# Kernel tuning notes

Measured on AMD Instinct MI355X. Metric: run time of the kernel, lower is better.

Reference implementation:

```python
import jax, jax.numpy as jnp
import numpy as np

D_MODEL = 256
N_HEAD = 8
D_FF = 2048
B, N = 8, 1024
NEG = -9e15
EPS = 1e-5


def _layernorm(x, g, b):
    mu = jnp.mean(x, axis=-1, keepdims=True)
    var = jnp.mean(jnp.square(x - mu), axis=-1, keepdims=True)
    return (x - mu) * jax.lax.rsqrt(var + EPS) * g + b


def setup_inputs() -> dict:
    key = jax.random.key(0)
    ks = jax.random.split(key, 12)
    d, dff = D_MODEL, D_FF
    s = 1.0 / np.sqrt(d)
    inp = {
        "src": jax.random.normal(ks[0], (B, N, d), dtype=jnp.float32),
        "adj": jax.random.randint(ks[1], (B, N, N), 0, 2, dtype=jnp.int32),
        "W_gat": jax.random.normal(ks[2], (d, d), dtype=jnp.float32) * s,
        "a_gat": jax.random.normal(ks[3], (2 * d, 1), dtype=jnp.float32) * s,
        "in_proj_w": jax.random.normal(ks[4], (3 * d, d), dtype=jnp.float32) * s,
        "in_proj_b": jnp.zeros((3 * d,), dtype=jnp.float32),
        "out_proj_w": jax.random.normal(ks[5], (d, d), dtype=jnp.float32) * s,
        "out_proj_b": jnp.zeros((d,), dtype=jnp.float32),
        "lin1_w": jax.random.normal(ks[6], (dff, d), dtype=jnp.float32) * s,
        "lin1_b": jnp.zeros((dff,), dtype=jnp.float32),
        "lin2_w": jax.random.normal(ks[7], (d, dff), dtype=jnp.float32) * (1.0 / np.sqrt(dff)),
        "lin2_b": jnp.zeros((d,), dtype=jnp.float32),
        "ln1_g": jnp.ones((d,), dtype=jnp.float32),
        "ln1_b": jnp.zeros((d,), dtype=jnp.float32),
        "ln2_g": jnp.ones((d,), dtype=jnp.float32),
        "ln2_b": jnp.zeros((d,), dtype=jnp.float32),
        "ln3_g": jnp.ones((d,), dtype=jnp.float32),
        "ln3_b": jnp.zeros((d,), dtype=jnp.float32),
    }
    return inp


def reference(src, adj, W_gat, a_gat, in_proj_w, in_proj_b, out_proj_w, out_proj_b,
              lin1_w, lin1_b, lin2_w, lin2_b, ln1_g, ln1_b, ln2_g, ln2_b, ln3_g, ln3_b):
    d = D_MODEL
    # --- Graph attention (dropout inactive in eval) ---
    Wh = jnp.matmul(src, W_gat)                      # [B,N,d]
    a1 = a_gat[:d, 0]
    a2 = a_gat[d:, 0]
    # e[b,i,j] = Wh_i . a1 + Wh_j . a2  (equivalent to concat+matmul in source)
    f1 = Wh @ a1                                     # [B,N]
    f2 = Wh @ a2                                     # [B,N]
    e = f1[:, :, None] + f2[:, None, :]              # [B,N,N]
    e = jnp.where(adj > 0, e, NEG)
    attn = jax.nn.softmax(e, axis=-1)
    h_prime = jnp.matmul(attn, Wh)                   # [B,N,d]
    graph_out = jax.nn.elu(h_prime)
    x = _layernorm(src + graph_out, ln1_g, ln1_b)

    # --- Multi-head self-attention ---
    qkv = x @ in_proj_w.T + in_proj_b                # [B,N,3d]
    q, k, v = jnp.split(qkv, 3, axis=-1)
    hd = d // N_HEAD
    def heads(t):
        return t.reshape(B, N, N_HEAD, hd).transpose(0, 2, 1, 3)  # [B,H,N,hd]
    q, k, v = heads(q), heads(k), heads(v)
    scores = jnp.einsum("bhid,bhjd->bhij", q, k) / np.sqrt(hd)
    probs = jax.nn.softmax(scores, axis=-1)
    ctx = jnp.einsum("bhij,bhjd->bhid", probs, v)
    ctx = ctx.transpose(0, 2, 1, 3).reshape(B, N, d)
    attn_out = ctx @ out_proj_w.T + out_proj_b
    y = _layernorm(x + attn_out, ln2_g, ln2_b)

    # --- FFN ---
    ff = jax.nn.relu(y @ lin1_w.T + lin1_b) @ lin2_w.T + lin2_b
    return _layernorm(y + ff, ln3_g, ln3_b)
```

## Files before the change

kernel.cpp:

```cpp
#include <hip/hip_runtime.h>
#include <math.h>

constexpr int BATCH = 8;
constexpr int SEQ   = 1024;
constexpr int DM    = 256;
constexpr int DF    = 2048;
constexpr int NH    = 8;
constexpr int HDIM  = 32;
constexpr int ROWS  = BATCH * SEQ;
constexpr float NEGV = -9e15f;
constexpr float EPSV = 1e-5f;
constexpr float QSCALE = 0.2550351822f;
constexpr float LOG2E  = 1.44269504f;

typedef __attribute__((ext_vector_type(8))) short short8;
typedef __attribute__((ext_vector_type(4))) float f32x4;

static __device__ __forceinline__ ushort f2bf(float f) {
    unsigned x = __float_as_uint(f);
    unsigned r = (x + 0x7fffu + ((x >> 16) & 1u)) >> 16;
    return (ushort)r;
}
static __device__ __forceinline__ unsigned cvt_pk_bf16(float lo, float hi) {
    unsigned r;
    asm volatile("v_cvt_pk_bf16_f32 %0, %1, %2" : "=v"(r) : "v"(lo), "v"(hi));
    return r;
}
static __device__ __forceinline__ void gl16(const ushort* g, ushort* l) {
    __builtin_amdgcn_global_load_lds(
        (const __attribute__((address_space(1))) void*)g,
        (__attribute__((address_space(3))) void*)l, 16, 0, 0);
}

struct CastArgs {
    const float* in[5];
    ushort* out[5];
    int n4[5];
};
__global__ __launch_bounds__(256) void castall_k(CastArgs a)
{
    int idx = blockIdx.x * 256 + threadIdx.x;
    #pragma unroll
    for (int r = 0; r < 5; r++) {
        if (idx < a.n4[r]) {
            float4 v = *(const float4*)&a.in[r][(size_t)idx * 4];
            ushort4 o; o.x = f2bf(v.x); o.y = f2bf(v.y); o.z = f2bf(v.z); o.w = f2bf(v.w);
            *(ushort4*)&a.out[r][(size_t)idx * 4] = o;
            return;
        }
        idx -= a.n4[r];
    }
}

__global__ __launch_bounds__(256) void tcast_k(const float* __restrict__ In,
                                               ushort* __restrict__ Out,
                                               int R, int C)
{
    __shared__ float Ts[32][33];
    const int r0 = blockIdx.y * 32, c0 = blockIdx.x * 32;
    const int t = threadIdx.x;
    const int lr = t >> 3, lc4 = (t & 7) * 4;
    float4 v = *(const float4*)&In[(size_t)(r0 + lr) * C + c0 + lc4];
    Ts[lr][lc4] = v.x; Ts[lr][lc4 + 1] = v.y; Ts[lr][lc4 + 2] = v.z; Ts[lr][lc4 + 3] = v.w;
    __syncthreads();
    const int oc = t >> 3, or4 = (t & 7) * 4;
    ushort4 o;
    o.x = f2bf(Ts[or4 + 0][oc]); o.y = f2bf(Ts[or4 + 1][oc]);
    o.z = f2bf(Ts[or4 + 2][oc]); o.w = f2bf(Ts[or4 + 3][oc]);
    *(ushort4*)&Out[(size_t)(c0 + oc) * R + r0 + or4] = o;
}

__global__ __launch_bounds__(256) void w12_k(const float* __restrict__ W_gat,
                                             const float* __restrict__ a_gat,
                                             float* __restrict__ w1,
                                             float* __restrict__ w2)
{
    const int t = threadIdx.x;
    const int k = blockIdx.x * 4 + (t >> 6);
    const int l = t & 63;
    float4 wv = *(const float4*)&W_gat[(size_t)k * DM + 4 * l];
    float4 a1 = *(const float4*)&a_gat[4 * l];
    float4 a2 = *(const float4*)&a_gat[DM + 4 * l];
    float s1 = wv.x*a1.x + wv.y*a1.y + wv.z*a1.z + wv.w*a1.w;
    float s2 = wv.x*a2.x + wv.y*a2.y + wv.z*a2.z + wv.w*a2.w;
    #pragma unroll
    for (int off = 32; off; off >>= 1) {
        s1 += __shfl_xor(s1, off, 64);
        s2 += __shfl_xor(s2, off, 64);
    }
    if (l == 0) { w1[k] = s1; w2[k] = s2; }
}

__global__ __launch_bounds__(256) void f12_k(const float* __restrict__ src,
                                             const float* __restrict__ w1,
                                             const float* __restrict__ w2,
                                             float* __restrict__ f1,
                                             float* __restrict__ f2)
{
    const int t = threadIdx.x;
    const size_t row = (size_t)blockIdx.x * 4 + (t >> 6);
    const int l = t & 63;
    float s1 = 0.f, s2 = 0.f;
    #pragma unroll
    for (int i = 0; i < 4; i++) {
        float v = src[row * DM + l + 64*i];
        s1 = fmaf(v, w1[l + 64*i], s1);
        s2 = fmaf(v, w2[l + 64*i], s2);
    }
    #pragma unroll
    for (int off = 32; off; off >>= 1) {
        s1 += __shfl_xor(s1, off, 64);
        s2 += __shfl_xor(s2, off, 64);
    }
    if (l == 0) { f1[row] = s1 * LOG2E; f2[row] = s2 * LOG2E; }
}

template<int EP, int BM, int BN>
__global__ __launch_bounds__(256) void gemm_bf(const ushort* __restrict__ A,
                                               const ushort* __restrict__ B,
                                               const float* __restrict__ bias,
                                               float* __restrict__ Cf,
                                               ushort* __restrict__ Cb,
                                               int M, int N, int K, int ldB,
                                               long long sA, long long sB, long long sC)
{
    __shared__ ushort As[2][BM][32];
    __shared__ ushort Bs[2][BN][32];
    A += (size_t)blockIdx.z * sA;
    B += (size_t)blockIdx.z * sB;

    const int t  = threadIdx.x;
    const int m0 = blockIdx.y * BM, n0 = blockIdx.x * BN;
    const int lane = t & 63, lo = lane & 15, hi = lane >> 4;
    const int w = t >> 6;
    constexpr int NI = BM / 32, NJ = BN / 32;
    const int wr = (w >> 1) * (BM / 2);
    const int wc = (w & 1) * (BN / 2);

    const int lr16 = lane >> 2;
    const int lc8  = (lane & 3) * 8;

    f32x4 acc[NI][NJ];
    const f32x4 zero = {0.f, 0.f, 0.f, 0.f};
    #pragma unroll
    for (int i = 0; i < NI; i++)
        #pragma unroll
        for (int j = 0; j < NJ; j++) acc[i][j] = zero;

    auto stage = [&](int buf, int k0) {
        if constexpr (BM == 128) {
            gl16(A + (size_t)(m0 + 32*w      + lr16) * K + k0 + lc8, &As[buf][32*w][0]);
            gl16(A + (size_t)(m0 + 32*w + 16 + lr16) * K + k0 + lc8, &As[buf][32*w + 16][0]);
        } else {
            gl16(A + (size_t)(m0 + 16*w + lr16) * K + k0 + lc8, &As[buf][16*w][0]);
        }
        if constexpr (BN == 128) {
            gl16(B + (size_t)(n0 + 32*w      + lr16) * ldB + k0 + lc8, &Bs[buf][32*w][0]);
            gl16(B + (size_t)(n0 + 32*w + 16 + lr16) * ldB + k0 + lc8, &Bs[buf][32*w + 16][0]);
        } else {
            gl16(B + (size_t)(n0 + 16*w + lr16) * ldB + k0 + lc8, &Bs[buf][16*w][0]);
        }
    };

    stage(0, 0);
    const int NT = K >> 5;
    for (int it = 0; it < NT; it++) {
        const int cur = it & 1;
        __syncthreads();
        if (it + 1 < NT) stage(cur ^ 1, (it + 1) << 5);

        short8 afr[NI], bfr[NJ];
        #pragma unroll
        for (int i = 0; i < NI; i++) afr[i] = *(const short8*)&As[cur][wr + i*16 + lo][hi * 8];
        #pragma unroll
        for (int j = 0; j < NJ; j++) bfr[j] = *(const short8*)&Bs[cur][wc + j*16 + lo][hi * 8];
        #pragma unroll
        for (int i = 0; i < NI; i++)
            #pragma unroll
            for (int j = 0; j < NJ; j++)
                acc[i][j] = __builtin_amdgcn_mfma_f32_16x16x32_bf16(afr[i], bfr[j], acc[i][j], 0, 0, 0);
    }

    if (EP == 2 || EP == 5 || EP == 6) Cb += (size_t)blockIdx.z * sC;
    else                               Cf += (size_t)blockIdx.z * sC;
    #pragma unroll
    for (int j = 0; j < NJ; j++) {
        const int col = n0 + wc + j * 16 + lo;
        float bj = (EP == 1 || EP == 2 || EP == 6) ? bias[col] : 0.f;
        #pragma unroll
        for (int i = 0; i < NI; i++) {
            const int rbase = m0 + wr + i * 16 + hi * 4;
            #pragma unroll
            for (int r = 0; r < 4; r++) {
                float v = acc[i][j][r] + bj;
                if (EP == 3) v = v > 0.f ? v : expm1f(v);
                if (EP == 2) v = fmaxf(v, 0.f);
                if (EP == 6 && col < DM) v *= QSCALE;
                if (EP == 2 || EP == 5 || EP == 6) Cb[(size_t)(rbase + r) * N + col] = f2bf(v);
                else                               Cf[(size_t)(rbase + r) * N + col] = v;
            }
        }
    }
}

template<bool WB>
__global__ __launch_bounds__(256) void ln_k(const float* __restrict__ a,
                                            const float* __restrict__ r,
                                            const float* __restrict__ g,
                                            const float* __restrict__ be,
                                            float* __restrict__ o,
                                            ushort* __restrict__ ob)
{
    const size_t row = (size_t)blockIdx.x * 4 + (threadIdx.x >> 6);
    const int l = threadIdx.x & 63;
    const float* pa = a + row * DM;
    const float* pr = r + row * DM;
    float v[4]; float s = 0.f;
    #pragma unroll
    for (int i = 0; i < 4; i++) { v[i] = pa[l + 64*i] + pr[l + 64*i]; s += v[i]; }
    #pragma unroll
    for (int off = 32; off; off >>= 1) s += __shfl_xor(s, off, 64);
    float mu = s * (1.0f / DM);
    float q = 0.f;
    #pragma unroll
    for (int i = 0; i < 4; i++) { float d = v[i] - mu; q += d * d; }
    #pragma unroll
    for (int off = 32; off; off >>= 1) q += __shfl_xor(q, off, 64);
    float rs = rsqrtf(q * (1.0f / DM) + EPSV);
    #pragma unroll
    for (int i = 0; i < 4; i++) {
        int c = l + 64*i;
        float out = (v[i] - mu) * rs * g[c] + be[c];
        o[row * DM + c] = out;
        if (WB) ob[row * DM + c] = f2bf(out);
    }
}

__global__ __launch_bounds__(256) void gat_sm_k(const int* __restrict__ adj,
                                                const float* __restrict__ f1,
                                                const float* __restrict__ f2,
                                                ushort* __restrict__ P)
{
    __shared__ float red[8];
    const int i = blockIdx.x, b = i >> 10;
    const int t = threadIdx.x;
    const int4 a4 = *(const int4*)&adj[(size_t)i * SEQ + 4 * t];
    const float4 f4 = *(const float4*)&f2[(size_t)(b << 10) + 4 * t];
    const float f1i = f1[i];
    float e[4];
    e[0] = a4.x > 0 ? f1i + f4.x : NEGV;
    e[1] = a4.y > 0 ? f1i + f4.y : NEGV;
    e[2] = a4.z > 0 ? f1i + f4.z : NEGV;
    e[3] = a4.w > 0 ? f1i + f4.w : NEGV;
    float mx = fmaxf(fmaxf(e[0], e[1]), fmaxf(e[2], e[3]));
    #pragma unroll
    for (int off = 32; off; off >>= 1) mx = fmaxf(mx, __shfl_xor(mx, off, 64));
    if ((t & 63) == 0) red[t >> 6] = mx;
    __syncthreads();
    mx = fmaxf(fmaxf(red[0], red[1]), fmaxf(red[2], red[3]));
    float s = 0.f;
    #pragma unroll
    for (int u = 0; u < 4; u++) { e[u] = exp2f(e[u] - mx); s += e[u]; }
    #pragma unroll
    for (int off = 32; off; off >>= 1) s += __shfl_xor(s, off, 64);
    if ((t & 63) == 0) red[4 + (t >> 6)] = s;
    __syncthreads();
    float inv = 1.0f / (red[4] + red[5] + red[6] + red[7]);
    ushort4 o;
    o.x = f2bf(e[0] * inv); o.y = f2bf(e[1] * inv);
    o.z = f2bf(e[2] * inv); o.w = f2bf(e[3] * inv);
    *(ushort4*)&P[(size_t)i * SEQ + 4 * t] = o;
}

__device__ __forceinline__ int vt_idx(int d, int kv) { return d * 72 + ((d >> 3) & 3) * 16 + kv; }
constexpr int VTSZ = 32 * 72 + 3 * 16 + 8;

__global__ __launch_bounds__(256) void mha_k(const ushort* __restrict__ qkv,
                                             ushort* __restrict__ ctxb)
{
    __shared__ ushort Ks[2][64][40];
    __shared__ ushort Vt[2][VTSZ];
    __shared__ ushort Ps[64][72];

    const int blk = blockIdx.x;
    const int qt = blk & 15, h = (blk >> 4) & 7, b = blk >> 7;
    const int i0 = qt << 6;
    const int t = threadIdx.x;
    const int w = t >> 6, lane = t & 63, lo = lane & 15, hi = lane >> 4;
    const int gsh = lane & 48;
    const size_t base = (size_t)b * SEQ * 768;

    const short8 aQ = *(const short8*)(qkv + base + (size_t)(i0 + 16*w + lo) * 768 + h * HDIM + hi * 8);
    short8 ones;
    #pragma unroll
    for (int e = 0; e < 8; e++) ones[e] = (short)0x3F80;

    const int srow = t >> 2, scb = (t & 3) << 3;
    const int vcol = (srow & 32) | ((srow & 15) << 1) | ((srow >> 4) & 1);
    {
        const ushort* p0 = qkv + base + (size_t)srow * 768 + h * HDIM;
        short8 k0 = *(const short8*)(p0 + 256 + scb);
        short8 v0 = *(const short8*)(p0 + 512 + scb);
        *(short8*)&Ks[0][srow][scb] = k0;
        #pragma unroll
        for (int e = 0; e < 8; e++) Vt[0][vt_idx(scb + e, vcol)] = (ushort)v0[e];
    }

    float m_run[4], l_run[4];
    f32x4 O0 = {0.f, 0.f, 0.f, 0.f}, O1 = {0.f, 0.f, 0.f, 0.f};
    #pragma unroll
    for (int r = 0; r < 4; r++) { m_run[r] = -3.0e38f; l_run[r] = 0.f; }
    const f32x4 zero = {0.f, 0.f, 0.f, 0.f};

    short8 kreg, vreg;
    for (int it = 0; it < 16; it++) {
        const int cur = it & 1;
        if (it < 15) {
            const ushort* nb = qkv + base + (size_t)((it + 1) * 64 + srow) * 768 + h * HDIM;
            kreg = *(const short8*)(nb + 256 + scb);
            vreg = *(const short8*)(nb + 512 + scb);
        }
        __syncthreads();

        f32x4 S[4];
        #pragma unroll
        for (int jt = 0; jt < 4; jt++) {
            short8 bK = *(const short8*)&Ks[cur][16 * jt + lo][hi * 8];
            S[jt] = __builtin_amdgcn_mfma_f32_16x16x32_bf16(aQ, bK, zero, 0, 0, 0);
        }

        float mxl[4];
        bool any = false;
        #pragma unroll
        for (int r = 0; r < 4; r++) {
            mxl[r] = fmaxf(fmaxf(S[0][r], S[1][r]), fmaxf(S[2][r], S[3][r]));
            any = any || (mxl[r] > m_run[r] + 8.f);
        }
        unsigned long long bal = __ballot(any);
        if ((bal >> gsh) & 0xffffULL) {
            #pragma unroll
            for (int r = 0; r < 4; r++) {
                float mx = mxl[r];
                #pragma unroll
                for (int off = 8; off; off >>= 1) mx = fmaxf(mx, __shfl_xor(mx, off, 16));
                float mnew = fmaxf(m_run[r], mx);
                float sc = exp2f(m_run[r] - mnew);
                m_run[r] = mnew;
                l_run[r] *= sc; O0[r] *= sc; O1[r] *= sc;
            }
        }
        #pragma unroll
        for (int r = 0; r < 4; r++) {
            const int row = 16 * w + 4 * hi + r;
            unsigned u01 = cvt_pk_bf16(exp2f(S[0][r] - m_run[r]), exp2f(S[1][r] - m_run[r]));
            unsigned u23 = cvt_pk_bf16(exp2f(S[2][r] - m_run[r]), exp2f(S[3][r] - m_run[r]));
            *(unsigned*)&Ps[row][2 * lo]      = u01;
            *(unsigned*)&Ps[row][32 + 2 * lo] = u23;
        }

        f32x4 O2 = zero;
        #pragma unroll
        for (int kt = 0; kt < 2; kt++) {
            short8 aP  = *(const short8*)&Ps[16 * w + lo][32 * kt + hi * 8];
            short8 bV0 = *(const short8*)&Vt[cur][vt_idx(lo,      32 * kt + hi * 8)];
            short8 bV1 = *(const short8*)&Vt[cur][vt_idx(16 + lo, 32 * kt + hi * 8)];
            O0 = __builtin_amdgcn_mfma_f32_16x16x32_bf16(aP, bV0, O0, 0, 0, 0);
            O1 = __builtin_amdgcn_mfma_f32_16x16x32_bf16(aP, bV1, O1, 0, 0, 0);
            O2 = __builtin_amdgcn_mfma_f32_16x16x32_bf16(aP, ones, O2, 0, 0, 0);
        }
        #pragma unroll
        for (int r = 0; r < 4; r++) l_run[r] += O2[r];

        if (it < 15) {
            *(short8*)&Ks[cur ^ 1][srow][scb] = kreg;
            #pragma unroll
            for (int e = 0; e < 8; e++) Vt[cur ^ 1][vt_idx(scb + e, vcol)] = (ushort)vreg[e];
        }
    }

    #pragma unroll
    for (int r = 0; r < 4; r++) {
        float inv = 1.0f / l_run[r];
        size_t row = (size_t)b * SEQ + i0 + 16 * w + 4 * hi + r;
        ctxb[row * DM + h * HDIM + lo]      = f2bf(O0[r] * inv);
        ctxb[row * DM + h * HDIM + 16 + lo] = f2bf(O1[r] * inv);
    }
}

extern "C" void kernel_launch(void* const* d_in, const int* in_sizes, int n_in,
                              void* d_out, int out_size, void* d_ws, size_t ws_size,
                              hipStream_t stream)
{
    const float* src        = (const float*)d_in[0];
    const int*   adj        = (const int*)  d_in[1];
    const float* W_gat      = (const float*)d_in[2];
    const float* a_gat      = (const float*)d_in[3];
    const float* in_proj_w  = (const float*)d_in[4];
    const float* in_proj_b  = (const float*)d_in[5];
    const float* out_proj_w = (const float*)d_in[6];
    const float* out_proj_b = (const float*)d_in[7];
    const float* lin1_w     = (const float*)d_in[8];
    const float* lin1_b     = (const float*)d_in[9];
    const float* lin2_w     = (const float*)d_in[10];
    const float* lin2_b     = (const float*)d_in[11];
    const float* ln1_g      = (const float*)d_in[12];
    const float* ln1_b_     = (const float*)d_in[13];
    const float* ln2_g      = (const float*)d_in[14];
    const float* ln2_b_     = (const float*)d_in[15];
    const float* ln3_g      = (const float*)d_in[16];
    const float* ln3_b_     = (const float*)d_in[17];

    char* base = (char*)d_ws;
    const size_t MB = 1024 * 1024;
    float*  tmp   = (float*) (base + 0 * MB);
    float*  x     = (float*) (base + 8 * MB);
    float*  y     = (float*) (base + 16 * MB);
    ushort* P_bf  = (ushort*)(base + 24 * MB);
    ushort* qkvb  = (ushort*)(base + 24 * MB);
    ushort* ff1b  = (ushort*)(base + 24 * MB);
    ushort* srcb  = (ushort*)(base + 56 * MB);
    ushort* WhTb  = (ushort*)(base + 60 * MB);
    ushort* xb    = (ushort*)(base + 64 * MB);
    ushort* yb    = (ushort*)(base + 68 * MB);
    ushort* ctxb  = (ushort*)(base + 72 * MB);
    float*  f1    = (float*) (base + 76 * MB);
    float*  f2    = f1 + ROWS;
    float*  w1    = f2 + ROWS;
    float*  w2    = w1 + DM;
    ushort* wgTb  = (ushort*)(base + 77 * MB);
    ushort* ipwb  = wgTb + 65536;
    ushort* opwb  = ipwb + 196608;
    ushort* l1wb  = opwb + 65536;
    ushort* l2wb  = l1wb + 524288;

    dim3 b256(256);

    CastArgs ca;
    ca.in[0] = src;       ca.out[0] = srcb; ca.n4[0] = 2097152 / 4;
    ca.in[1] = in_proj_w; ca.out[1] = ipwb; ca.n4[1] = 196608 / 4;
    ca.in[2] = out_proj_w;ca.out[2] = opwb; ca.n4[2] = 65536 / 4;
    ca.in[3] = lin1_w;    ca.out[3] = l1wb; ca.n4[3] = 524288 / 4;
    ca.in[4] = lin2_w;    ca.out[4] = l2wb; ca.n4[4] = 524288 / 4;
    castall_k<<<(2097152 + 196608 + 65536 + 524288 + 524288) / 4 / 256, b256, 0, stream>>>(ca);
    tcast_k<<<dim3(8, 8), b256, 0, stream>>>(W_gat, wgTb, 256, 256);

    w12_k<<<64, b256, 0, stream>>>(W_gat, a_gat, w1, w2);
    f12_k<<<ROWS / 4, b256, 0, stream>>>(src, w1, w2, f1, f2);
    gemm_bf<5, 64, 64><<<dim3(ROWS/64, DM/64, 1), b256, 0, stream>>>(wgTb, srcb, nullptr, nullptr, WhTb,
                                                                     DM, ROWS, DM, DM, 0, 0, 0);
    gat_sm_k<<<ROWS, b256, 0, stream>>>(adj, f1, f2, P_bf);
    gemm_bf<3, 64, 64><<<dim3(DM/64, SEQ/64, 8), b256, 0, stream>>>(P_bf, WhTb, nullptr, tmp, nullptr,
                                                                    SEQ, DM, SEQ, ROWS,
                                                                    (long long)SEQ * SEQ, (long long)SEQ, (long long)SEQ * DM);
    ln_k<true><<<ROWS / 4, b256, 0, stream>>>(src, tmp, ln1_g, ln1_b_, x, xb);

    gemm_bf<6, 128, 64><<<dim3(768/64, ROWS/128, 1), b256, 0, stream>>>(xb, ipwb, in_proj_b, nullptr, qkvb,
                                                                        ROWS, 768, DM, DM, 0, 0, 0);
    mha_k<<<BATCH * NH * (SEQ / 64), b256, 0, stream>>>(qkvb, ctxb);
    gemm_bf<1, 64, 64><<<dim3(DM/64, ROWS/64, 1), b256, 0, stream>>>(ctxb, opwb, out_proj_b, tmp, nullptr,
                                                                     ROWS, DM, DM, DM, 0, 0, 0);
    ln_k<true><<<ROWS / 4, b256, 0, stream>>>(x, tmp, ln2_g, ln2_b_, y, yb);

    gemm_bf<2, 128, 128><<<dim3(DF/128, ROWS/128, 1), b256, 0, stream>>>(yb, l1wb, lin1_b, nullptr, ff1b,
                                                                         ROWS, DF, DM, DM, 0, 0, 0);
    gemm_bf<1, 64, 64><<<dim3(DM/64, ROWS/64, 1), b256, 0, stream>>>(ff1b, l2wb, lin2_b, tmp, nullptr,
                                                                     ROWS, DM, DF, DF, 0, 0, 0);
    ln_k<false><<<ROWS / 4, b256, 0, stream>>>(y, tmp, ln3_g, ln3_b_, (float*)d_out, nullptr);
}
```

Measured before the change: 169.4 us.

## Fuse residual-add LayerNorm into epilogues of N=256 GEMMs

Adds a gemm_ln_k kernel in which each block computes a full 32x256 output row-tile, stages it through shared memory, then applies the bias/ELU, residual add and LayerNorm in place. It replaces the three GEMM + separate ln_k pairs: GAT aggregation, out-projection and FFN down-projection. This removes the fp32 tmp round-trip and three launches. The trade-off is far fewer blocks (256 per launch) and a larger shared-memory footprint, so the K=2048 FFN down-projection in particular may lose parallelism.

```diff
diff --git a/kernel.cpp b/kernel.cpp
--- a/kernel.cpp
+++ b/kernel.cpp
@@ -119,15 +119,11 @@
 __global__ __launch_bounds__(256) void gemm_bf(const ushort* __restrict__ A,
                                                const ushort* __restrict__ B,
                                                const float* __restrict__ bias,
-                                               float* __restrict__ Cf,
                                                ushort* __restrict__ Cb,
-                                               int M, int N, int K, int ldB,
-                                               long long sA, long long sB, long long sC)
+                                               int N, int K, int ldB)
 {
     __shared__ ushort As[2][BM][32];
     __shared__ ushort Bs[2][BN][32];
-    A += (size_t)blockIdx.z * sA;
-    B += (size_t)blockIdx.z * sB;
 
     const int t  = threadIdx.x;
     const int m0 = blockIdx.y * BM, n0 = blockIdx.x * BN;
@@ -181,58 +177,147 @@
                 acc[i][j] = __builtin_amdgcn_mfma_f32_16x16x32_bf16(afr[i], bfr[j], acc[i][j], 0, 0, 0);
     }
 
-    if (EP == 2 || EP == 5 || EP == 6) Cb += (size_t)blockIdx.z * sC;
-    else                               Cf += (size_t)blockIdx.z * sC;
     #pragma unroll
     for (int j = 0; j < NJ; j++) {
         const int col = n0 + wc + j * 16 + lo;
-        float bj = (EP == 1 || EP == 2 || EP == 6) ? bias[col] : 0.f;
+        float bj = (EP == 2 || EP == 6) ? bias[col] : 0.f;
         #pragma unroll
         for (int i = 0; i < NI; i++) {
             const int rbase = m0 + wr + i * 16 + hi * 4;
             #pragma unroll
             for (int r = 0; r < 4; r++) {
                 float v = acc[i][j][r] + bj;
-                if (EP == 3) v = v > 0.f ? v : expm1f(v);
                 if (EP == 2) v = fmaxf(v, 0.f);
                 if (EP == 6 && col < DM) v *= QSCALE;
-                if (EP == 2 || EP == 5 || EP == 6) Cb[(size_t)(rbase + r) * N + col] = f2bf(v);
-                else                               Cf[(size_t)(rbase + r) * N + col] = v;
+                Cb[(size_t)(rbase + r) * N + col] = f2bf(v);
             }
         }
     }
 }
 
-template<bool WB>
-__global__ __launch_bounds__(256) void ln_k(const float* __restrict__ a,
-                                            const float* __restrict__ r,
-                                            const float* __restrict__ g,
-                                            const float* __restrict__ be,
-                                            float* __restrict__ o,
-                                            ushort* __restrict__ ob)
-{
-    const size_t row = (size_t)blockIdx.x * 4 + (threadIdx.x >> 6);
-    const int l = threadIdx.x & 63;
-    const float* pa = a + row * DM;
-    const float* pr = r + row * DM;
-    float v[4]; float s = 0.f;
-    #pragma unroll
-    for (int i = 0; i < 4; i++) { v[i] = pa[l + 64*i] + pr[l + 64*i]; s += v[i]; }
-    #pragma unroll
-    for (int off = 32; off; off >>= 1) s += __shfl_xor(s, off, 64);
-    float mu = s * (1.0f / DM);
-    float q = 0.f;
-    #pragma unroll
-    for (int i = 0; i < 4; i++) { float d = v[i] - mu; q += d * d; }
-    #pragma unroll
-    for (int off = 32; off; off >>= 1) q += __shfl_xor(q, off, 64);
-    float rs = rsqrtf(q * (1.0f / DM) + EPSV);
-    #pragma unroll
-    for (int i = 0; i < 4; i++) {
-        int c = l + 64*i;
-        float out = (v[i] - mu) * rs * g[c] + be[c];
-        o[row * DM + c] = out;
-        if (WB) ob[row * DM + c] = f2bf(out);
+template<int ACT, bool WB>
+__global__ __launch_bounds__(256) void gemm_ln_k(const ushort* __restrict__ A,
+                                                 const ushort* __restrict__ B,
+                                                 const float* __restrict__ bias,
+                                                 const float* __restrict__ resid,
+                                                 const float* __restrict__ g,
+                                                 const float* __restrict__ be,
+                                                 float* __restrict__ outF,
+                                                 ushort* __restrict__ outB,
+                                                 int K, int ldB,
+                                                 long long sA, long long sB, long long sR)
+{
+    union U {
+        struct { ushort As[2][32][32]; ushort Bs[2][256][32]; } s;
+        float vals[32][264];
+    };
+    __shared__ U u;
+
+    A     += (size_t)blockIdx.z * sA;
+    B     += (size_t)blockIdx.z * sB;
+    resid += (size_t)blockIdx.z * sR;
+    outF  += (size_t)blockIdx.z * sR;
+    if (WB) outB += (size_t)blockIdx.z * sR;
+
+    const int t = threadIdx.x;
+    const int m0 = blockIdx.y * 32;
+    const int lane = t & 63, lo = lane & 15, hi = lane >> 4;
+    const int w = t >> 6;
+    const int lr16 = lane >> 2, lc8 = (lane & 3) * 8;
+
+    f32x4 acc[2][4];
+    const f32x4 zero = {0.f, 0.f, 0.f, 0.f};
+    #pragma unroll
+    for (int i = 0; i < 2; i++)
+        #pragma unroll
+        for (int j = 0; j < 4; j++) acc[i][j] = zero;
+
+    auto stage = [&](int buf, int k0) {
+        if (w < 2)
+            gl16(A + (size_t)(m0 + 16*w + lr16) * K + k0 + lc8, &u.s.As[buf][16*w][0]);
+        #pragma unroll
+        for (int j = 0; j < 4; j++)
+            gl16(B + (size_t)(j*64 + 16*w + lr16) * ldB + k0 + lc8, &u.s.Bs[buf][j*64 + 16*w][0]);
+    };
+
+    stage(0, 0);
+    const int NT = K >> 5;
+    for (int it = 0; it < NT; it++) {
+        const int cur = it & 1;
+        __syncthreads();
+        if (it + 1 < NT) stage(cur ^ 1, (it + 1) << 5);
+
+        short8 afr[2], bfr[4];
+        #pragma unroll
+        for (int i = 0; i < 2; i++) afr[i] = *(const short8*)&u.s.As[cur][i*16 + lo][hi * 8];
+        #pragma unroll
+        for (int j = 0; j < 4; j++) bfr[j] = *(const short8*)&u.s.Bs[cur][64*w + j*16 + lo][hi * 8];
+        #pragma unroll
+        for (int i = 0; i < 2; i++)
+            #pragma unroll
+            for (int j = 0; j < 4; j++)
+                acc[i][j] = __builtin_amdgcn_mfma_f32_16x16x32_bf16(afr[i], bfr[j], acc[i][j], 0, 0, 0);
+    }
+
+    __syncthreads();
+
+    #pragma unroll
+    for (int j = 0; j < 4; j++) {
+        const int col = 64*w + j*16 + lo;
+        float bj = (ACT == 1) ? bias[col] : 0.f;
+        #pragma unroll
+        for (int i = 0; i < 2; i++) {
+            const int rbase = i*16 + hi*4;
+            #pragma unroll
+            for (int r = 0; r < 4; r++) {
+                float v = acc[i][j][r] + bj;
+                if (ACT == 0) v = v > 0.f ? v : expm1f(v);
+                u.vals[rbase + r][col] = v;
+            }
+        }
+    }
+    __syncthreads();
+
+    const int row = t >> 3, s = t & 7;
+    const float* rrow = resid + (size_t)(m0 + row) * DM + s * 32;
+    float vv[32];
+    float sum = 0.f;
+    #pragma unroll
+    for (int q = 0; q < 8; q++) {
+        float4 rv = *(const float4*)(rrow + 4*q);
+        vv[4*q+0] = u.vals[row][s*32 + 4*q + 0] + rv.x;
+        vv[4*q+1] = u.vals[row][s*32 + 4*q + 1] + rv.y;
+        vv[4*q+2] = u.vals[row][s*32 + 4*q + 2] + rv.z;
+        vv[4*q+3] = u.vals[row][s*32 + 4*q + 3] + rv.w;
+        sum += (vv[4*q] + vv[4*q+1]) + (vv[4*q+2] + vv[4*q+3]);
+    }
+    #pragma unroll
+    for (int off = 1; off < 8; off <<= 1) sum += __shfl_xor(sum, off, 8);
+    const float mu = sum * (1.0f / DM);
+    float qs = 0.f;
+    #pragma unroll
+    for (int k = 0; k < 32; k++) { float d = vv[k] - mu; qs += d * d; }
+    #pragma unroll
+    for (int off = 1; off < 8; off <<= 1) qs += __shfl_xor(qs, off, 8);
+    const float rs = rsqrtf(qs * (1.0f / DM) + EPSV);
+
+    float* orow = outF + (size_t)(m0 + row) * DM + s * 32;
+    #pragma unroll
+    for (int q = 0; q < 8; q++) {
+        const int c = s*32 + 4*q;
+        float4 gv = *(const float4*)&g[c];
+        float4 bv = *(const float4*)&be[c];
+        float4 o;
+        o.x = (vv[4*q+0] - mu) * rs * gv.x + bv.x;
+        o.y = (vv[4*q+1] - mu) * rs * gv.y + bv.y;
+        o.z = (vv[4*q+2] - mu) * rs * gv.z + bv.z;
+        o.w = (vv[4*q+3] - mu) * rs * gv.w + bv.w;
+        *(float4*)(orow + 4*q) = o;
+        if (WB) {
+            ushort4 ob;
+            ob.x = f2bf(o.x); ob.y = f2bf(o.y); ob.z = f2bf(o.z); ob.w = f2bf(o.w);
+            *(ushort4*)&outB[(size_t)(m0 + row) * DM + c] = ob;
+        }
     }
 }
 
@@ -412,22 +497,21 @@
 
     char* base = (char*)d_ws;
     const size_t MB = 1024 * 1024;
-    float*  tmp   = (float*) (base + 0 * MB);
-    float*  x     = (float*) (base + 8 * MB);
-    float*  y     = (float*) (base + 16 * MB);
-    ushort* P_bf  = (ushort*)(base + 24 * MB);
-    ushort* qkvb  = (ushort*)(base + 24 * MB);
-    ushort* ff1b  = (ushort*)(base + 24 * MB);
-    ushort* srcb  = (ushort*)(base + 56 * MB);
-    ushort* WhTb  = (ushort*)(base + 60 * MB);
-    ushort* xb    = (ushort*)(base + 64 * MB);
-    ushort* yb    = (ushort*)(base + 68 * MB);
-    ushort* ctxb  = (ushort*)(base + 72 * MB);
-    float*  f1    = (float*) (base + 76 * MB);
+    float*  x     = (float*) (base + 0 * MB);
+    float*  y     = (float*) (base + 8 * MB);
+    ushort* P_bf  = (ushort*)(base + 16 * MB);
+    ushort* qkvb  = (ushort*)(base + 16 * MB);
+    ushort* ff1b  = (ushort*)(base + 16 * MB);
+    ushort* srcb  = (ushort*)(base + 48 * MB);
+    ushort* WhTb  = (ushort*)(base + 52 * MB);
+    ushort* xb    = (ushort*)(base + 56 * MB);
+    ushort* yb    = (ushort*)(base + 60 * MB);
+    ushort* ctxb  = (ushort*)(base + 64 * MB);
+    float*  f1    = (float*) (base + 68 * MB);
     float*  f2    = f1 + ROWS;
     float*  w1    = f2 + ROWS;
     float*  w2    = w1 + DM;
-    ushort* wgTb  = (ushort*)(base + 77 * MB);
+    ushort* wgTb  = (ushort*)(base + 69 * MB);
     ushort* ipwb  = wgTb + 65536;
     ushort* opwb  = ipwb + 196608;
     ushort* l1wb  = opwb + 65536;
@@ -446,24 +530,24 @@
 
     w12_k<<<64, b256, 0, stream>>>(W_gat, a_gat, w1, w2);
     f12_k<<<ROWS / 4, b256, 0, stream>>>(src, w1, w2, f1, f2);
-    gemm_bf<5, 64, 64><<<dim3(ROWS/64, DM/64, 1), b256, 0, stream>>>(wgTb, srcb, nullptr, nullptr, WhTb,
-                                                                     DM, ROWS, DM, DM, 0, 0, 0);
+    gemm_bf<5, 64, 64><<<dim3(ROWS/64, DM/64, 1), b256, 0, stream>>>(wgTb, srcb, nullptr, WhTb,
+                                                                     ROWS, DM, DM);
     gat_sm_k<<<ROWS, b256, 0, stream>>>(adj, f1, f2, P_bf);
-    gemm_bf<3, 64, 64><<<dim3(DM/64, SEQ/64, 8), b256, 0, stream>>>(P_bf, WhTb, nullptr, tmp, nullptr,
-                                                                    SEQ, DM, SEQ, ROWS,
-                                                                    (long long)SEQ * SEQ, (long long)SEQ, (long long)SEQ * DM);
-    ln_k<true><<<ROWS / 4, b256, 0, stream>>>(src, tmp, ln1_g, ln1_b_, x, xb);
-
-    gemm_bf<6, 128, 64><<<dim3(768/64, ROWS/128, 1), b256, 0, stream>>>(xb, ipwb, in_proj_b, nullptr, qkvb,
-                                                                        ROWS, 768, DM, DM, 0, 0, 0);
+    gemm_ln_k<0, true><<<dim3(1, SEQ/32, 8), b256, 0, stream>>>(P_bf, WhTb, nullptr,
+                                                                src, ln1_g, ln1_b_, x, xb,
+                                                                SEQ, ROWS,
+                                                                (long long)SEQ * SEQ, (long long)SEQ, (long long)SEQ * DM);
+
+    gemm_bf<6, 128, 64><<<dim3(768/64, ROWS/128, 1), b256, 0, stream>>>(xb, ipwb, in_proj_b, qkvb,
+                                                                        768, DM, DM);
     mha_k<<<BATCH * NH * (SEQ / 64), b256, 0, stream>>>(qkvb, ctxb);
-    gemm_bf<1, 64, 64><<<dim3(DM/64, ROWS/64, 1), b256, 0, stream>>>(ctxb, opwb, out_proj_b, tmp, nullptr,
-                                                                     ROWS, DM, DM, DM, 0, 0, 0);
-    ln_k<true><<<ROWS / 4, b256, 0, stream>>>(x, tmp, ln2_g, ln2_b_, y, yb);
-
-    gemm_bf<2, 128, 128><<<dim3(DF/128, ROWS/128, 1), b256, 0, stream>>>(yb, l1wb, lin1_b, nullptr, ff1b,
-                                                                         ROWS, DF, DM, DM, 0, 0, 0);
-    gemm_bf<1, 64, 64><<<dim3(DM/64, ROWS/64, 1), b256, 0, stream>>>(ff1b, l2wb, lin2_b, tmp, nullptr,
-                                                                     ROWS, DM, DF, DF, 0, 0, 0);
-    ln_k<false><<<ROWS / 4, b256, 0, stream>>>(y, tmp, ln3_g, ln3_b_, (float*)d_out, nullptr);
-}
+    gemm_ln_k<1, true><<<dim3(1, ROWS/32, 1), b256, 0, stream>>>(ctxb, opwb, out_proj_b,
+                                                                 x, ln2_g, ln2_b_, y, yb,
+                                                                 DM, DM, 0, 0, 0);
+
+    gemm_bf<2, 128, 128><<<dim3(DF/128, ROWS/128, 1), b256, 0, stream>>>(yb, l1wb, lin1_b, ff1b,
+                                                                         DF, DM, DM);
+    gemm_ln_k<1, false><<<dim3(1, ROWS/32, 1), b256, 0, stream>>>(ff1b, l2wb, lin2_b,
+                                                                  y, ln3_g, ln3_b_, (float*)d_out, nullptr,
+                                                                  DF, DF, 0, 0, 0);
+}
```

Result: slower. 236.2 us (+39.4%).
